# Kernel optimization log

Hardware: AMD Instinct MI355X
Metric: run time of the kernel (lower is better)

The kernel has to match this reference:

```python
import jax, jax.numpy as jnp
import numpy as np

N_NODES = 100_000
N_EDGES = 1_600_000
D_IN, D_HID, N_CLASSES = 128, 128, 40


def setup_inputs() -> dict:
    key = jax.random.key(0)
    ks = jax.random.split(key, 8)
    x = jax.random.normal(ks[0], (N_NODES, D_IN), dtype=jnp.float32)
    edge_index = jax.random.randint(ks[1], (2, N_EDGES), 0, N_NODES, dtype=jnp.int64)
    dims = [(D_IN, D_HID), (D_HID, D_HID), (D_HID, N_CLASSES)]
    inp = {"x": x, "edge_index": edge_index}
    for i, (di, do) in enumerate(dims):
        s = 1.0 / np.sqrt(di)
        inp[f"W_l{i}"] = jax.random.normal(ks[2 + 2 * i], (di, do), dtype=jnp.float32) * s
        inp[f"W_r{i}"] = jax.random.normal(ks[3 + 2 * i], (di, do), dtype=jnp.float32) * s
        inp[f"b{i}"] = jnp.zeros((do,), dtype=jnp.float32)
    return inp


def _sage_conv(x, src, dst, deg_inv, W_l, W_r, b):
    # gather messages from source nodes, mean-aggregate at target nodes
    msg = x[src]                                        # [E, d_in]
    aggr = jax.ops.segment_sum(msg, dst, num_segments=N_NODES) * deg_inv  # [N, d_in]
    return aggr @ W_l + b + x @ W_r                     # [N, d_out]


def reference(x, edge_index, W_l0, W_r0, b0, W_l1, W_r1, b1, W_l2, W_r2, b2):
    src, dst = edge_index[0], edge_index[1]
    deg = jax.ops.segment_sum(jnp.ones((N_EDGES,), x.dtype), dst, num_segments=N_NODES)
    deg_inv = (1.0 / jnp.maximum(deg, 1.0))[:, None]    # [N, 1]

    h = _sage_conv(x, src, dst, deg_inv, W_l0, W_r0, b0)
    h = jax.nn.relu(h)  # dropout p=0.3 is identity in eval mode
    h = _sage_conv(h, src, dst, deg_inv, W_l1, W_r1, b1)
    h = jax.nn.relu(h)
    h = _sage_conv(h, src, dst, deg_inv, W_l2, W_r2, b2)
    return jax.nn.log_softmax(h, axis=1)
```

## Files before the change

### kernel.cpp

```cpp
#include <hip/hip_runtime.h>
#include <math.h>

#define THREADS 256
#define BSHIFT 8
#define BSIZE 256
#define NEB 512

typedef short short8 __attribute__((ext_vector_type(8)));
typedef float f32x4 __attribute__((ext_vector_type(4)));

__device__ __forceinline__ unsigned short f2bf(float f) {
  unsigned u = __builtin_bit_cast(unsigned, f);
  return (unsigned short)((u + 0x7FFFu + ((u >> 16) & 1u)) >> 16);
}
__device__ __forceinline__ float bflo(unsigned u) {
  return __builtin_bit_cast(float, u << 16);
}
__device__ __forceinline__ float bfhi(unsigned u) {
  return __builtin_bit_cast(float, u & 0xFFFF0000u);
}
__device__ __forceinline__ unsigned pack2(float x, float y) {
  return (unsigned)f2bf(x) | ((unsigned)f2bf(y) << 16);
}

__device__ __forceinline__ void acc8(float* a, uint4 u) {
  a[0] += bflo(u.x); a[1] += bfhi(u.x);
  a[2] += bflo(u.y); a[3] += bfhi(u.y);
  a[4] += bflo(u.z); a[5] += bfhi(u.z);
  a[6] += bflo(u.w); a[7] += bfhi(u.w);
}


__global__ __launch_bounds__(256) void k_ehist(const int* __restrict__ dst,
                                               int* __restrict__ cnt_bm,
                                               int E, int chunk, int nbk) {
  __shared__ int h[1024];
  int blk = blockIdx.x, t = threadIdx.x;
  for (int i = t; i < nbk; i += 256) h[i] = 0;
  __syncthreads();
  int e0 = blk * chunk, e1 = min(e0 + chunk, E);
  for (int e = e0 + t; e < e1; e += 256) atomicAdd(&h[dst[e] >> BSHIFT], 1);
  __syncthreads();
  for (int i = t; i < nbk; i += 256) cnt_bm[(size_t)blk * nbk + i] = h[i];
}

__global__ __launch_bounds__(256) void k_bktscan(const int* __restrict__ cnt_bm,
                                                 int* __restrict__ locoff_tm,
                                                 int* __restrict__ bktot, int nbk) {
  int g = blockIdx.x, t = threadIdx.x;
  int c0 = cnt_bm[(size_t)(2 * t) * nbk + g];
  int c1 = cnt_bm[(size_t)(2 * t + 1) * nbk + g];
  __shared__ int sh[256];
  int s = c0 + c1;
  sh[t] = s;
  __syncthreads();
  for (int off = 1; off < 256; off <<= 1) {
    int v = (t >= off) ? sh[t - off] : 0;
    __syncthreads();
    if (t >= off) sh[t] += v;
    __syncthreads();
  }
  int excl = sh[t] - s;
  ((int2*)(locoff_tm + (size_t)g * NEB))[t] = make_int2(excl, excl + c0);
  if (t == 255) bktot[g] = sh[255];
}

__global__ __launch_bounds__(256) void k_topscan(const int* __restrict__ bktot,
                                                 int* __restrict__ bucket_base,
                                                 int nbk, int E,
                                                 int* __restrict__ row_ptr, int N) {
  __shared__ int sums[256];
  int t = threadIdx.x;
  int vals[4];
  int s = 0;
#pragma unroll
  for (int j = 0; j < 4; ++j) {
    int idx = t * 4 + j;
    vals[j] = (idx < nbk) ? bktot[idx] : 0;
    s += vals[j];
  }
  sums[t] = s;
  __syncthreads();
  for (int off = 1; off < 256; off <<= 1) {
    int v = (t >= off) ? sums[t - off] : 0;
    __syncthreads();
    if (t >= off) sums[t] += v;
    __syncthreads();
  }
  int run = sums[t] - s;
#pragma unroll
  for (int j = 0; j < 4; ++j) {
    int idx = t * 4 + j;
    if (idx < nbk) bucket_base[idx] = run;
    run += vals[j];
  }
  if (t == 0) { bucket_base[nbk] = E; row_ptr[N] = E; }
}

__global__ __launch_bounds__(256) void k_eplace(const int* __restrict__ src,
                                                const int* __restrict__ dst,
                                                const int* __restrict__ bucket_base,
                                                const int* __restrict__ locoff_tm,
                                                int* __restrict__ bedge,
                                                int E, int chunk, int nbk) {
  __shared__ int lptr[1024];
  int blk = blockIdx.x, t = threadIdx.x;
  for (int i = t; i < nbk; i += 256)
    lptr[i] = bucket_base[i] + locoff_tm[(size_t)i * NEB + blk];
  __syncthreads();
  int e0 = blk * chunk, e1 = min(e0 + chunk, E);
  for (int e = e0 + t; e < e1; e += 256) {
    int d = dst[e];
    int b = d >> BSHIFT;
    int p = atomicAdd(&lptr[b], 1);
    bedge[p] = (src[e] << 8) | (d & (BSIZE - 1));
  }
}

__global__ __launch_bounds__(256) void k_bcsr2(const int* __restrict__ bedge,
                                               const int* __restrict__ bucket_base,
                                               int* __restrict__ row_ptr,
                                               int* __restrict__ col, int N) {
  int g = blockIdx.x, t = threadIdx.x;
  int beg = bucket_base[g], end = bucket_base[g + 1];
  __shared__ int deg[BSIZE];
  __shared__ int sh[BSIZE];
  __shared__ int cur[BSIZE];
  deg[t] = 0;
  __syncthreads();
  for (int i = beg + t; i < end; i += 256)
    atomicAdd(&deg[bedge[i] & (BSIZE - 1)], 1);
  __syncthreads();
  int s = deg[t];
  sh[t] = s;
  __syncthreads();
  for (int off = 1; off < 256; off <<= 1) {
    int v = (t >= off) ? sh[t - off] : 0;
    __syncthreads();
    if (t >= off) sh[t] += v;
    __syncthreads();
  }
  int ex = beg + sh[t] - s;
  int node = g * BSIZE + t;
  if (node < N) row_ptr[node] = ex;
  cur[t] = ex;
  __syncthreads();
  for (int i = beg + t; i < end; i += 256) {
    int ed = bedge[i];
    int p = atomicAdd(&cur[ed & (BSIZE - 1)], 1);
    col[p] = ed >> 8;
  }
}

__global__ __launch_bounds__(256) void k_wswz_all(
    const float* __restrict__ Wl0, const float* __restrict__ Wr0,
    const float* __restrict__ Wl1, const float* __restrict__ Wr1,
    const float* __restrict__ Wl2, const float* __restrict__ Wr2,
    unsigned short* __restrict__ out0, unsigned short* __restrict__ out1,
    unsigned short* __restrict__ out2) {
  int b = blockIdx.x, t = threadIdx.x;
  if (b < 256) {
    const float* Wl = (b < 128) ? Wl0 : Wl1;
    const float* Wr = (b < 128) ? Wr0 : Wr1;
    unsigned short* out = (b < 128) ? out0 : out1;
    int idx = (b & 127) * 256 + t;
    int j = idx & 7, lane = (idx >> 3) & 63, ct = (idx >> 9) & 15, ks = idx >> 13;
    int k = ks * 32 + (lane >> 4) * 8 + j;
    int c = ct * 16 + (lane & 15);
    float v = (c < 128) ? Wl[k * 128 + c] : Wr[k * 128 + (c - 128)];
    out[idx] = f2bf(v);
  } else {
    int idx = (b - 256) * 256 + t;
    int j = idx & 7, lane = (idx >> 3) & 63;
    int tile = idx >> 9;
    int ct = tile % 5, ks = tile / 5;
    int k = ks * 32 + (lane >> 4) * 8 + j;
    int c = ct * 16 + (lane & 15);
    float v = (c < 40) ? Wl2[k * 40 + c] : ((c < 80) ? Wr2[k * 40 + (c - 40)] : 0.f);
    out2[idx] = f2bf(v);
  }
}

__global__ __launch_bounds__(256) void gemm128_mfma_x32(
    const float* __restrict__ X, const unsigned short* __restrict__ Wswz,
    const float* __restrict__ bias,
    unsigned short* __restrict__ outL, unsigned short* __restrict__ outR, int M) {
  int wave = threadIdx.x >> 6, lane = threadIdx.x & 63;
  int quad = lane >> 4, n16 = lane & 15;
  int rowA = blockIdx.x * 128 + wave * 16 + n16;
  int rowB = rowA + 64;
  int rA = min(rowA, M - 1), rB = min(rowB, M - 1);
  bool okA = rowA < M, okB = rowB < M;

  short8 xf[4], xg[4];
  const float* xpA = X + (size_t)rA * 128 + quad * 8;
  const float* xpB = X + (size_t)rB * 128 + quad * 8;
#pragma unroll
  for (int ks = 0; ks < 4; ++ks) {
    float4 a0 = *(const float4*)(xpA + ks * 32);
    float4 a1 = *(const float4*)(xpA + ks * 32 + 4);
    float4 b0 = *(const float4*)(xpB + ks * 32);
    float4 b1 = *(const float4*)(xpB + ks * 32 + 4);
    short8 f, g;
    f[0] = (short)f2bf(a0.x); f[1] = (short)f2bf(a0.y);
    f[2] = (short)f2bf(a0.z); f[3] = (short)f2bf(a0.w);
    f[4] = (short)f2bf(a1.x); f[5] = (short)f2bf(a1.y);
    f[6] = (short)f2bf(a1.z); f[7] = (short)f2bf(a1.w);
    g[0] = (short)f2bf(b0.x); g[1] = (short)f2bf(b0.y);
    g[2] = (short)f2bf(b0.z); g[3] = (short)f2bf(b0.w);
    g[4] = (short)f2bf(b1.x); g[5] = (short)f2bf(b1.y);
    g[6] = (short)f2bf(b1.z); g[7] = (short)f2bf(b1.w);
    xf[ks] = f;
    xg[ks] = g;
  }

  size_t obA = (size_t)rowA * 128, obB = (size_t)rowB * 128;
#pragma unroll 2
  for (int ct = 0; ct < 16; ++ct) {
    f32x4 accA = {0.f, 0.f, 0.f, 0.f};
    f32x4 accB = {0.f, 0.f, 0.f, 0.f};
    const unsigned short* wp = Wswz + (size_t)(ct * 64 + lane) * 8;
#pragma unroll
    for (int ks = 0; ks < 4; ++ks) {
      short8 wf = *(const short8*)(wp + ks * 8192);
      accA = __builtin_amdgcn_mfma_f32_16x16x32_bf16(wf, xf[ks], accA, 0, 0, 0);
      accB = __builtin_amdgcn_mfma_f32_16x16x32_bf16(wf, xg[ks], accB, 0, 0, 0);
    }
    int colh = (ct & 7) * 16 + quad * 4;
    if (ct < 8) {
      if (okA) {
        ushort4 o;
        o.x = f2bf(accA[0]); o.y = f2bf(accA[1]); o.z = f2bf(accA[2]); o.w = f2bf(accA[3]);
        *(ushort4*)(outL + obA + colh) = o;
      }
      if (okB) {
        ushort4 o;
        o.x = f2bf(accB[0]); o.y = f2bf(accB[1]); o.z = f2bf(accB[2]); o.w = f2bf(accB[3]);
        *(ushort4*)(outL + obB + colh) = o;
      }
    } else {
      float4 bv = *(const float4*)(bias + colh);
      if (okA) {
        ushort4 o;
        o.x = f2bf(accA[0] + bv.x); o.y = f2bf(accA[1] + bv.y);
        o.z = f2bf(accA[2] + bv.z); o.w = f2bf(accA[3] + bv.w);
        *(ushort4*)(outR + obA + colh) = o;
      }
      if (okB) {
        ushort4 o;
        o.x = f2bf(accB[0] + bv.x); o.y = f2bf(accB[1] + bv.y);
        o.z = f2bf(accB[2] + bv.z); o.w = f2bf(accB[3] + bv.w);
        *(ushort4*)(outR + obB + colh) = o;
      }
    }
  }
}

__global__ __launch_bounds__(256) void gemm128_mfma(
    const unsigned short* __restrict__ Xb, const unsigned short* __restrict__ Wswz,
    const float* __restrict__ bias,
    unsigned short* __restrict__ outL, unsigned short* __restrict__ outR, int M) {
  int wave = threadIdx.x >> 6, lane = threadIdx.x & 63;
  int quad = lane >> 4, n16 = lane & 15;
  int rowA = blockIdx.x * 128 + wave * 16 + n16;
  int rowB = rowA + 64;
  int rA = min(rowA, M - 1), rB = min(rowB, M - 1);
  bool okA = rowA < M, okB = rowB < M;

  short8 xf[4], xg[4];
  const unsigned short* xpA = Xb + (size_t)rA * 128 + quad * 8;
  const unsigned short* xpB = Xb + (size_t)rB * 128 + quad * 8;
#pragma unroll
  for (int ks = 0; ks < 4; ++ks) {
    xf[ks] = *(const short8*)(xpA + ks * 32);
    xg[ks] = *(const short8*)(xpB + ks * 32);
  }

  size_t obA = (size_t)rowA * 128, obB = (size_t)rowB * 128;
#pragma unroll 2
  for (int ct = 0; ct < 16; ++ct) {
    f32x4 accA = {0.f, 0.f, 0.f, 0.f};
    f32x4 accB = {0.f, 0.f, 0.f, 0.f};
    const unsigned short* wp = Wswz + (size_t)(ct * 64 + lane) * 8;
#pragma unroll
    for (int ks = 0; ks < 4; ++ks) {
      short8 wf = *(const short8*)(wp + ks * 8192);
      accA = __builtin_amdgcn_mfma_f32_16x16x32_bf16(wf, xf[ks], accA, 0, 0, 0);
      accB = __builtin_amdgcn_mfma_f32_16x16x32_bf16(wf, xg[ks], accB, 0, 0, 0);
    }
    int colh = (ct & 7) * 16 + quad * 4;
    if (ct < 8) {
      if (okA) {
        ushort4 o;
        o.x = f2bf(accA[0]); o.y = f2bf(accA[1]); o.z = f2bf(accA[2]); o.w = f2bf(accA[3]);
        *(ushort4*)(outL + obA + colh) = o;
      }
      if (okB) {
        ushort4 o;
        o.x = f2bf(accB[0]); o.y = f2bf(accB[1]); o.z = f2bf(accB[2]); o.w = f2bf(accB[3]);
        *(ushort4*)(outL + obB + colh) = o;
      }
    } else {
      float4 bv = *(const float4*)(bias + colh);
      if (okA) {
        ushort4 o;
        o.x = f2bf(accA[0] + bv.x); o.y = f2bf(accA[1] + bv.y);
        o.z = f2bf(accA[2] + bv.z); o.w = f2bf(accA[3] + bv.w);
        *(ushort4*)(outR + obA + colh) = o;
      }
      if (okB) {
        ushort4 o;
        o.x = f2bf(accB[0] + bv.x); o.y = f2bf(accB[1] + bv.y);
        o.z = f2bf(accB[2] + bv.z); o.w = f2bf(accB[3] + bv.w);
        *(ushort4*)(outR + obB + colh) = o;
      }
    }
  }
}

__global__ __launch_bounds__(256) void gemm40_mfma(
    const unsigned short* __restrict__ Xb, const unsigned short* __restrict__ Wswz,
    const float* __restrict__ bias,
    unsigned short* __restrict__ tlb, float* __restrict__ tr, int M) {
  int wave = threadIdx.x >> 6, lane = threadIdx.x & 63;
  int quad = lane >> 4, n16 = lane & 15;
  int row = blockIdx.x * 64 + wave * 16 + n16;
  int row_ld = min(row, M - 1);
  bool ok = row < M;

  short8 xf[4];
  const unsigned short* xp = Xb + (size_t)row_ld * 128 + quad * 8;
#pragma unroll
  for (int ks = 0; ks < 4; ++ks) xf[ks] = *(const short8*)(xp + ks * 32);

#pragma unroll
  for (int ct = 0; ct < 5; ++ct) {
    f32x4 acc = {0.f, 0.f, 0.f, 0.f};
    const unsigned short* wp = Wswz + (size_t)(ct * 64 + lane) * 8;
#pragma unroll
    for (int ks = 0; ks < 4; ++ks) {
      short8 wf = *(const short8*)(wp + (size_t)ks * 5 * 64 * 8);
      acc = __builtin_amdgcn_mfma_f32_16x16x32_bf16(wf, xf[ks], acc, 0, 0, 0);
    }
    int cglob = ct * 16 + quad * 4;
    if (!ok) continue;
    if (cglob < 40) {
      ushort4 o;
      o.x = f2bf(acc[0]); o.y = f2bf(acc[1]); o.z = f2bf(acc[2]); o.w = f2bf(acc[3]);
      *(ushort4*)(tlb + (size_t)row * 64 + cglob) = o;
    } else {
      int c = cglob - 40;
      float4 bv = *(const float4*)(bias + c);
      float4 o;
      o.x = acc[0] + bv.x; o.y = acc[1] + bv.y;
      o.z = acc[2] + bv.z; o.w = acc[3] + bv.w;
      *(float4*)(tr + (size_t)row * 40 + c) = o;
    }
  }
}

__global__ __launch_bounds__(256) void agg128b(
    const unsigned short* __restrict__ xl, const unsigned short* __restrict__ xr,
    const int* __restrict__ row_ptr, const int* __restrict__ col,
    unsigned short* __restrict__ h, int Nn) {
  int wave = threadIdx.x >> 6;
  int lane = threadIdx.x & 63;
  int pair = lane >> 5;
  int l32 = lane & 31;
  int n = blockIdx.x * 4 + wave;
  if (n >= Nn) return;
  int beg = row_ptr[n], end = row_ptr[n + 1];
  int deg = end - beg;
  const uint2* xlq = (const uint2*)xl;
  float a0x = 0.f, a0y = 0.f, a0z = 0.f, a0w = 0.f;
  float a1x = 0.f, a1y = 0.f, a1z = 0.f, a1w = 0.f;
  float a2x = 0.f, a2y = 0.f, a2z = 0.f, a2w = 0.f;
  float a3x = 0.f, a3y = 0.f, a3z = 0.f, a3w = 0.f;
  int e = beg + pair;
  for (int it = deg >> 3; it > 0; --it, e += 8) {
    uint2 u0 = xlq[(size_t)col[e]     * 32 + l32];
    uint2 u1 = xlq[(size_t)col[e + 2] * 32 + l32];
    uint2 u2 = xlq[(size_t)col[e + 4] * 32 + l32];
    uint2 u3 = xlq[(size_t)col[e + 6] * 32 + l32];
    a0x += bflo(u0.x); a0y += bfhi(u0.x); a0z += bflo(u0.y); a0w += bfhi(u0.y);
    a1x += bflo(u1.x); a1y += bfhi(u1.x); a1z += bflo(u1.y); a1w += bfhi(u1.y);
    a2x += bflo(u2.x); a2y += bfhi(u2.x); a2z += bflo(u2.y); a2w += bfhi(u2.y);
    a3x += bflo(u3.x); a3y += bfhi(u3.x); a3z += bflo(u3.y); a3w += bfhi(u3.y);
  }
  for (; e < end; e += 2) {
    uint2 u = xlq[(size_t)col[e] * 32 + l32];
    a0x += bflo(u.x); a0y += bfhi(u.x); a0z += bflo(u.y); a0w += bfhi(u.y);
  }
  float ax = (a0x + a1x) + (a2x + a3x);
  float ay = (a0y + a1y) + (a2y + a3y);
  float az = (a0z + a1z) + (a2z + a3z);
  float aw = (a0w + a1w) + (a2w + a3w);
  ax += __shfl_xor(ax, 32);
  ay += __shfl_xor(ay, 32);
  az += __shfl_xor(az, 32);
  aw += __shfl_xor(aw, 32);
  if (pair == 0) {
    float di = 1.0f / (float)max(deg, 1);
    uint2 r = ((const uint2*)xr)[(size_t)n * 32 + l32];
    float ox = fmaxf(fmaf(ax, di, bflo(r.x)), 0.f);
    float oy = fmaxf(fmaf(ay, di, bfhi(r.x)), 0.f);
    float oz = fmaxf(fmaf(az, di, bflo(r.y)), 0.f);
    float ow = fmaxf(fmaf(aw, di, bfhi(r.y)), 0.f);
    uint2 o;
    o.x = pack2(ox, oy);
    o.y = pack2(oz, ow);
    ((uint2*)h)[(size_t)n * 32 + l32] = o;
  }
}

__global__ __launch_bounds__(256) void agg40_lsm(
    const unsigned short* __restrict__ tlb, const float* __restrict__ tr,
    const int* __restrict__ row_ptr, const int* __restrict__ col,
    float* __restrict__ out, int Nn) {
  int wave = threadIdx.x >> 6;
  int lane = threadIdx.x & 63;
  int ew = lane >> 3;
  int l8 = lane & 7;
  int n = blockIdx.x * 4 + wave;
  if (n >= Nn) return;
  int beg = row_ptr[n], end = row_ptr[n + 1];
  int deg = end - beg;
  const uint4* tlq = (const uint4*)tlb;
  float a0[8], a1[8];
#pragma unroll
  for (int j = 0; j < 8; ++j) { a0[j] = 0.f; a1[j] = 0.f; }
  int rounds = (deg + 15) >> 4;
  if (rounds > 0) {
    int end1 = end - 1;
    int e = beg + ew;
    int c0 = col[min(e, end1)];
    int c1 = col[min(e + 8, end1)];
    for (int it = rounds - 1; it > 0; --it) {
      uint4 u0 = tlq[(size_t)c0 * 8 + l8];
      uint4 u1 = tlq[(size_t)c1 * 8 + l8];
      int en = e + 16;
      int cn0 = col[min(en, end1)];
      int cn1 = col[min(en + 8, end1)];
      acc8(a0, u0); acc8(a1, u1);
      c0 = cn0; c1 = cn1; e = en;
    }
    uint4 u0 = tlq[(size_t)c0 * 8 + l8];
    uint4 u1 = tlq[(size_t)c1 * 8 + l8];
    uint4 z = make_uint4(0u, 0u, 0u, 0u);
    if (e >= end) u0 = z;
    if (e + 8 >= end) u1 = z;
    acc8(a0, u0); acc8(a1, u1);
  }
  float v[8];
#pragma unroll
  for (int j = 0; j < 8; ++j) {
    float t = a0[j] + a1[j];
    t += __shfl_xor(t, 32);
    t += __shfl_xor(t, 16);
    t += __shfl_xor(t, 8);
    v[j] = t;
  }
  bool valid = l8 < 5;
  float di = 1.0f / (float)max(deg, 1);
  float4 r0 = valid ? *(const float4*)(tr + (size_t)n * 40 + 8 * l8)
                    : make_float4(0.f, 0.f, 0.f, 0.f);
  float4 r1 = valid ? *(const float4*)(tr + (size_t)n * 40 + 8 * l8 + 4)
                    : make_float4(0.f, 0.f, 0.f, 0.f);
  float rb[8] = {r0.x, r0.y, r0.z, r0.w, r1.x, r1.y, r1.z, r1.w};
  float vv[8];
#pragma unroll
  for (int j = 0; j < 8; ++j) vv[j] = valid ? fmaf(v[j], di, rb[j]) : -INFINITY;
  float m = vv[0];
#pragma unroll
  for (int j = 1; j < 8; ++j) m = fmaxf(m, vv[j]);
#pragma unroll
  for (int off = 4; off; off >>= 1) m = fmaxf(m, __shfl_xor(m, off));
  float ex = 0.f;
  if (valid) {
#pragma unroll
    for (int j = 0; j < 8; ++j) ex += expf(vv[j] - m);
  }
  float ssum = ex;
#pragma unroll
  for (int off = 4; off; off >>= 1) ssum += __shfl_xor(ssum, off);
  float lg = logf(ssum);
  if (ew == 0 && valid) {
    float4 o0, o1;
    o0.x = (vv[0] - m) - lg; o0.y = (vv[1] - m) - lg;
    o0.z = (vv[2] - m) - lg; o0.w = (vv[3] - m) - lg;
    o1.x = (vv[4] - m) - lg; o1.y = (vv[5] - m) - lg;
    o1.z = (vv[6] - m) - lg; o1.w = (vv[7] - m) - lg;
    *(float4*)(out + (size_t)n * 40 + 8 * l8) = o0;
    *(float4*)(out + (size_t)n * 40 + 8 * l8 + 4) = o1;
  }
}


extern "C" void kernel_launch(void* const* d_in, const int* in_sizes, int n_in,
                              void* d_out, int out_size, void* d_ws, size_t ws_size,
                              hipStream_t stream) {
  const float* x   = (const float*)d_in[0];
  const int*   ei  = (const int*)d_in[1];
  const float* Wl0 = (const float*)d_in[2];
  const float* Wr0 = (const float*)d_in[3];
  const float* b0  = (const float*)d_in[4];
  const float* Wl1 = (const float*)d_in[5];
  const float* Wr1 = (const float*)d_in[6];
  const float* b1  = (const float*)d_in[7];
  const float* Wl2 = (const float*)d_in[8];
  const float* Wr2 = (const float*)d_in[9];
  const float* b2  = (const float*)d_in[10];

  int N = in_sizes[0] / 128;
  int E = in_sizes[1] / 2;
  const int* src = ei;
  const int* dst = ei + E;
  int nbk = (N + BSIZE - 1) / BSIZE;
  int chunk = (E + NEB - 1) / NEB;

  char* ws = (char*)d_ws;
  size_t off = 0;
  auto alloc = [&](size_t bytes) -> void* {
    void* p = ws + off;
    off += (bytes + 255) & ~(size_t)255;
    return p;
  };
  unsigned short* gA  = (unsigned short*)alloc((size_t)N * 128 * 2);
  unsigned short* gB  = (unsigned short*)alloc((size_t)N * 128 * 2);
  unsigned short* hC  = (unsigned short*)alloc((size_t)N * 128 * 2);
  unsigned short* tlb = (unsigned short*)alloc((size_t)N * 64 * 2);
  float* tr           = (float*)alloc((size_t)N * 40 * 4);
  int* row_ptr  = (int*)alloc((size_t)(N + 1) * 4);
  int* col      = (int*)alloc((size_t)E * 4);
  int* bedge    = (int*)alloc((size_t)E * 4);
  int* cnt_bm   = (int*)alloc((size_t)NEB * nbk * 4);
  int* locoff   = (int*)alloc((size_t)nbk * NEB * 4);
  int* bktot    = (int*)alloc((size_t)nbk * 4);
  int* bbase    = (int*)alloc((size_t)(nbk + 1) * 4);
  unsigned short* wswz0 = (unsigned short*)alloc(32768 * 2);
  unsigned short* wswz1 = (unsigned short*)alloc(32768 * 2);
  unsigned short* wswz2 = (unsigned short*)alloc(10240 * 2);
  (void)ws_size; (void)n_in; (void)out_size;

  k_ehist<<<NEB, 256, 0, stream>>>(dst, cnt_bm, E, chunk, nbk);
  k_bktscan<<<nbk, 256, 0, stream>>>(cnt_bm, locoff, bktot, nbk);
  k_topscan<<<1, 256, 0, stream>>>(bktot, bbase, nbk, E, row_ptr, N);
  k_eplace<<<NEB, 256, 0, stream>>>(src, dst, bbase, locoff, bedge, E, chunk, nbk);
  k_bcsr2<<<nbk, 256, 0, stream>>>(bedge, bbase, row_ptr, col, N);

  k_wswz_all<<<296, 256, 0, stream>>>(Wl0, Wr0, Wl1, Wr1, Wl2, Wr2,
                                      wswz0, wswz1, wswz2);

  int gg128 = (N + 127) / 128;
  int gg = (N + 63) / 64;
  int nb = (N + 3) / 4;

  gemm128_mfma_x32<<<gg128, 256, 0, stream>>>(x, wswz0, b0, gA, gB, N);
  agg128b<<<nb, 256, 0, stream>>>(gA, gB, row_ptr, col, hC, N);
  gemm128_mfma<<<gg128, 256, 0, stream>>>(hC, wswz1, b1, gA, gB, N);
  agg128b<<<nb, 256, 0, stream>>>(gA, gB, row_ptr, col, hC, N);
  gemm40_mfma<<<gg, 256, 0, stream>>>(hC, wswz2, b2, tlb, tr, N);
  agg40_lsm<<<nb, 256, 0, stream>>>(tlb, tr, row_ptr, col, (float*)d_out, N);
}
```

Measured before the change: 446.7 us.

## Store GEMM outputs in column-sliced layout and aggregate per 16-column slice

The GEMM kernels now write their bf16 outputs as 8 slices of 16 columns, each slice contiguous over all nodes (32 bytes per node per slice), rather than as row-major 128-column rows. The aggregation kernel launches 8 blocks per node group, one per slice. Each block gathers 16 edges at once with 4 lanes per edge and reduces them with shuffles. The aim is for each slice (about 3.2 MB) to stay resident in cache during the random neighbour gathers, which should improve hit rates. In exchange, each 32-byte gather is smaller, the column index and row_ptr are read 8 times, and the shuffle reduction is longer.

```diff
diff --git a/kernel.cpp b/kernel.cpp
--- a/kernel.cpp
+++ b/kernel.cpp
@@ -214,7 +214,6 @@
     xg[ks] = g;
   }
 
-  size_t obA = (size_t)rowA * 128, obB = (size_t)rowB * 128;
 #pragma unroll 2
   for (int ct = 0; ct < 16; ++ct) {
     f32x4 accA = {0.f, 0.f, 0.f, 0.f};
@@ -226,31 +225,32 @@
       accA = __builtin_amdgcn_mfma_f32_16x16x32_bf16(wf, xf[ks], accA, 0, 0, 0);
       accB = __builtin_amdgcn_mfma_f32_16x16x32_bf16(wf, xg[ks], accB, 0, 0, 0);
     }
-    int colh = (ct & 7) * 16 + quad * 4;
     if (ct < 8) {
+      size_t sbase = (size_t)ct * M;
       if (okA) {
         ushort4 o;
         o.x = f2bf(accA[0]); o.y = f2bf(accA[1]); o.z = f2bf(accA[2]); o.w = f2bf(accA[3]);
-        *(ushort4*)(outL + obA + colh) = o;
+        *(ushort4*)(outL + (sbase + rowA) * 16 + quad * 4) = o;
       }
       if (okB) {
         ushort4 o;
         o.x = f2bf(accB[0]); o.y = f2bf(accB[1]); o.z = f2bf(accB[2]); o.w = f2bf(accB[3]);
-        *(ushort4*)(outL + obB + colh) = o;
+        *(ushort4*)(outL + (sbase + rowB) * 16 + quad * 4) = o;
       }
     } else {
-      float4 bv = *(const float4*)(bias + colh);
+      size_t sbase = (size_t)(ct - 8) * M;
+      float4 bv = *(const float4*)(bias + (ct - 8) * 16 + quad * 4);
       if (okA) {
         ushort4 o;
         o.x = f2bf(accA[0] + bv.x); o.y = f2bf(accA[1] + bv.y);
         o.z = f2bf(accA[2] + bv.z); o.w = f2bf(accA[3] + bv.w);
-        *(ushort4*)(outR + obA + colh) = o;
+        *(ushort4*)(outR + (sbase + rowA) * 16 + quad * 4) = o;
       }
       if (okB) {
         ushort4 o;
         o.x = f2bf(accB[0] + bv.x); o.y = f2bf(accB[1] + bv.y);
         o.z = f2bf(accB[2] + bv.z); o.w = f2bf(accB[3] + bv.w);
-        *(ushort4*)(outR + obB + colh) = o;
+        *(ushort4*)(outR + (sbase + rowB) * 16 + quad * 4) = o;
       }
     }
   }
@@ -276,7 +276,6 @@
     xg[ks] = *(const short8*)(xpB + ks * 32);
   }
 
-  size_t obA = (size_t)rowA * 128, obB = (size_t)rowB * 128;
 #pragma unroll 2
   for (int ct = 0; ct < 16; ++ct) {
     f32x4 accA = {0.f, 0.f, 0.f, 0.f};
@@ -288,31 +287,32 @@
       accA = __builtin_amdgcn_mfma_f32_16x16x32_bf16(wf, xf[ks], accA, 0, 0, 0);
       accB = __builtin_amdgcn_mfma_f32_16x16x32_bf16(wf, xg[ks], accB, 0, 0, 0);
     }
-    int colh = (ct & 7) * 16 + quad * 4;
     if (ct < 8) {
+      size_t sbase = (size_t)ct * M;
       if (okA) {
         ushort4 o;
         o.x = f2bf(accA[0]); o.y = f2bf(accA[1]); o.z = f2bf(accA[2]); o.w = f2bf(accA[3]);
-        *(ushort4*)(outL + obA + colh) = o;
+        *(ushort4*)(outL + (sbase + rowA) * 16 + quad * 4) = o;
       }
       if (okB) {
         ushort4 o;
         o.x = f2bf(accB[0]); o.y = f2bf(accB[1]); o.z = f2bf(accB[2]); o.w = f2bf(accB[3]);
-        *(ushort4*)(outL + obB + colh) = o;
+        *(ushort4*)(outL + (sbase + rowB) * 16 + quad * 4) = o;
       }
     } else {
-      float4 bv = *(const float4*)(bias + colh);
+      size_t sbase = (size_t)(ct - 8) * M;
+      float4 bv = *(const float4*)(bias + (ct - 8) * 16 + quad * 4);
       if (okA) {
         ushort4 o;
         o.x = f2bf(accA[0] + bv.x); o.y = f2bf(accA[1] + bv.y);
         o.z = f2bf(accA[2] + bv.z); o.w = f2bf(accA[3] + bv.w);
-        *(ushort4*)(outR + obA + colh) = o;
+        *(ushort4*)(outR + (sbase + rowA) * 16 + quad * 4) = o;
       }
       if (okB) {
         ushort4 o;
         o.x = f2bf(accB[0] + bv.x); o.y = f2bf(accB[1] + bv.y);
         o.z = f2bf(accB[2] + bv.z); o.w = f2bf(accB[3] + bv.w);
-        *(ushort4*)(outR + obB + colh) = o;
+        *(ushort4*)(outR + (sbase + rowB) * 16 + quad * 4) = o;
       }
     }
   }
@@ -359,57 +359,51 @@
   }
 }
 
-__global__ __launch_bounds__(256) void agg128b(
-    const unsigned short* __restrict__ xl, const unsigned short* __restrict__ xr,
+__global__ __launch_bounds__(256) void agg128s(
+    const unsigned short* __restrict__ gAs, const unsigned short* __restrict__ gBs,
     const int* __restrict__ row_ptr, const int* __restrict__ col,
     unsigned short* __restrict__ h, int Nn) {
+  int bid = blockIdx.x;
+  int s = bid & 7;
+  int nblk = bid >> 3;
   int wave = threadIdx.x >> 6;
   int lane = threadIdx.x & 63;
-  int pair = lane >> 5;
-  int l32 = lane & 31;
-  int n = blockIdx.x * 4 + wave;
+  int es = lane >> 2;
+  int cl = lane & 3;
+  int n = nblk * 4 + wave;
   if (n >= Nn) return;
   int beg = row_ptr[n], end = row_ptr[n + 1];
   int deg = end - beg;
-  const uint2* xlq = (const uint2*)xl;
-  float a0x = 0.f, a0y = 0.f, a0z = 0.f, a0w = 0.f;
-  float a1x = 0.f, a1y = 0.f, a1z = 0.f, a1w = 0.f;
-  float a2x = 0.f, a2y = 0.f, a2z = 0.f, a2w = 0.f;
-  float a3x = 0.f, a3y = 0.f, a3z = 0.f, a3w = 0.f;
-  int e = beg + pair;
-  for (int it = deg >> 3; it > 0; --it, e += 8) {
-    uint2 u0 = xlq[(size_t)col[e]     * 32 + l32];
-    uint2 u1 = xlq[(size_t)col[e + 2] * 32 + l32];
-    uint2 u2 = xlq[(size_t)col[e + 4] * 32 + l32];
-    uint2 u3 = xlq[(size_t)col[e + 6] * 32 + l32];
-    a0x += bflo(u0.x); a0y += bfhi(u0.x); a0z += bflo(u0.y); a0w += bfhi(u0.y);
-    a1x += bflo(u1.x); a1y += bfhi(u1.x); a1z += bflo(u1.y); a1w += bfhi(u1.y);
-    a2x += bflo(u2.x); a2y += bfhi(u2.x); a2z += bflo(u2.y); a2w += bfhi(u2.y);
-    a3x += bflo(u3.x); a3y += bfhi(u3.x); a3z += bflo(u3.y); a3w += bfhi(u3.y);
-  }
-  for (; e < end; e += 2) {
-    uint2 u = xlq[(size_t)col[e] * 32 + l32];
-    a0x += bflo(u.x); a0y += bfhi(u.x); a0z += bflo(u.y); a0w += bfhi(u.y);
-  }
-  float ax = (a0x + a1x) + (a2x + a3x);
-  float ay = (a0y + a1y) + (a2y + a3y);
-  float az = (a0z + a1z) + (a2z + a3z);
-  float aw = (a0w + a1w) + (a2w + a3w);
-  ax += __shfl_xor(ax, 32);
-  ay += __shfl_xor(ay, 32);
-  az += __shfl_xor(az, 32);
-  aw += __shfl_xor(aw, 32);
-  if (pair == 0) {
+  const uint2* A = (const uint2*)gAs;
+  size_t sbase = (size_t)s * Nn;
+  float a0 = 0.f, a1 = 0.f, a2 = 0.f, a3 = 0.f;
+  int e = beg + es;
+  int end1 = end - 1;
+  for (int r = (deg + 15) >> 4; r > 0; --r, e += 16) {
+    int c = col[min(e, end1)];
+    uint2 u = A[(sbase + c) * 4 + cl];
+    if (e >= end) { u.x = 0u; u.y = 0u; }
+    a0 += bflo(u.x); a1 += bfhi(u.x); a2 += bflo(u.y); a3 += bfhi(u.y);
+  }
+  a0 += __shfl_xor(a0, 4);  a1 += __shfl_xor(a1, 4);
+  a2 += __shfl_xor(a2, 4);  a3 += __shfl_xor(a3, 4);
+  a0 += __shfl_xor(a0, 8);  a1 += __shfl_xor(a1, 8);
+  a2 += __shfl_xor(a2, 8);  a3 += __shfl_xor(a3, 8);
+  a0 += __shfl_xor(a0, 16); a1 += __shfl_xor(a1, 16);
+  a2 += __shfl_xor(a2, 16); a3 += __shfl_xor(a3, 16);
+  a0 += __shfl_xor(a0, 32); a1 += __shfl_xor(a1, 32);
+  a2 += __shfl_xor(a2, 32); a3 += __shfl_xor(a3, 32);
+  if (es == 0) {
     float di = 1.0f / (float)max(deg, 1);
-    uint2 r = ((const uint2*)xr)[(size_t)n * 32 + l32];
-    float ox = fmaxf(fmaf(ax, di, bflo(r.x)), 0.f);
-    float oy = fmaxf(fmaf(ay, di, bfhi(r.x)), 0.f);
-    float oz = fmaxf(fmaf(az, di, bflo(r.y)), 0.f);
-    float ow = fmaxf(fmaf(aw, di, bfhi(r.y)), 0.f);
+    uint2 rr = ((const uint2*)gBs)[(sbase + n) * 4 + cl];
+    float ox = fmaxf(fmaf(a0, di, bflo(rr.x)), 0.f);
+    float oy = fmaxf(fmaf(a1, di, bfhi(rr.x)), 0.f);
+    float oz = fmaxf(fmaf(a2, di, bflo(rr.y)), 0.f);
+    float ow = fmaxf(fmaf(a3, di, bfhi(rr.y)), 0.f);
     uint2 o;
     o.x = pack2(ox, oy);
     o.y = pack2(oz, ow);
-    ((uint2*)h)[(size_t)n * 32 + l32] = o;
+    ((uint2*)h)[(size_t)n * 32 + s * 4 + cl] = o;
   }
 }
 
@@ -553,12 +547,13 @@
 
   int gg128 = (N + 127) / 128;
   int gg = (N + 63) / 64;
+  int nb8 = 8 * ((N + 3) / 4);
   int nb = (N + 3) / 4;
 
   gemm128_mfma_x32<<<gg128, 256, 0, stream>>>(x, wswz0, b0, gA, gB, N);
-  agg128b<<<nb, 256, 0, stream>>>(gA, gB, row_ptr, col, hC, N);
+  agg128s<<<nb8, 256, 0, stream>>>(gA, gB, row_ptr, col, hC, N);
   gemm128_mfma<<<gg128, 256, 0, stream>>>(hC, wswz1, b1, gA, gB, N);
-  agg128b<<<nb, 256, 0, stream>>>(gA, gB, row_ptr, col, hC, N);
+  agg128s<<<nb8, 256, 0, stream>>>(gA, gB, row_ptr, col, hC, N);
   gemm40_mfma<<<gg, 256, 0, stream>>>(hC, wswz2, b2, tlb, tr, N);
   agg40_lsm<<<nb, 256, 0, stream>>>(tlb, tr, row_ptr, col, (float*)d_out, N);
 }
```

Result: slower. 719.4 us (+61.1%).

## Store GEMM outputs as column-sliced planes for aggregation gathers

Applied to the files above, without the earlier changes.

GEMM outputs (the gathered projection and the self term) move from row-major [N,128] bf16 to 16-column slabs laid out as [8][N][16], and the 40-class buffer becomes [5][N][16]. The aggregation kernels index by slab, so each gathered row is split across several separate 32-byte segments instead of one contiguous 256-byte row. The likely aim is better cache locality per column slab or more coalesced GEMM stores. The cost is that every random gather now touches several scattered segments, which could hurt DRAM and L2 efficiency.

```diff
diff --git a/kernel.cpp b/kernel.cpp
--- a/kernel.cpp
+++ b/kernel.cpp
@@ -214,7 +214,6 @@
     xg[ks] = g;
   }
 
-  size_t obA = (size_t)rowA * 128, obB = (size_t)rowB * 128;
 #pragma unroll 2
   for (int ct = 0; ct < 16; ++ct) {
     f32x4 accA = {0.f, 0.f, 0.f, 0.f};
@@ -226,31 +225,32 @@
       accA = __builtin_amdgcn_mfma_f32_16x16x32_bf16(wf, xf[ks], accA, 0, 0, 0);
       accB = __builtin_amdgcn_mfma_f32_16x16x32_bf16(wf, xg[ks], accB, 0, 0, 0);
     }
-    int colh = (ct & 7) * 16 + quad * 4;
     if (ct < 8) {
+      size_t sbase = (size_t)ct * M;
       if (okA) {
         ushort4 o;
         o.x = f2bf(accA[0]); o.y = f2bf(accA[1]); o.z = f2bf(accA[2]); o.w = f2bf(accA[3]);
-        *(ushort4*)(outL + obA + colh) = o;
+        *(ushort4*)(outL + (sbase + rowA) * 16 + quad * 4) = o;
       }
       if (okB) {
         ushort4 o;
         o.x = f2bf(accB[0]); o.y = f2bf(accB[1]); o.z = f2bf(accB[2]); o.w = f2bf(accB[3]);
-        *(ushort4*)(outL + obB + colh) = o;
+        *(ushort4*)(outL + (sbase + rowB) * 16 + quad * 4) = o;
       }
     } else {
-      float4 bv = *(const float4*)(bias + colh);
+      size_t sbase = (size_t)(ct - 8) * M;
+      float4 bv = *(const float4*)(bias + (ct - 8) * 16 + quad * 4);
       if (okA) {
         ushort4 o;
         o.x = f2bf(accA[0] + bv.x); o.y = f2bf(accA[1] + bv.y);
         o.z = f2bf(accA[2] + bv.z); o.w = f2bf(accA[3] + bv.w);
-        *(ushort4*)(outR + obA + colh) = o;
+        *(ushort4*)(outR + (sbase + rowA) * 16 + quad * 4) = o;
       }
       if (okB) {
         ushort4 o;
         o.x = f2bf(accB[0] + bv.x); o.y = f2bf(accB[1] + bv.y);
         o.z = f2bf(accB[2] + bv.z); o.w = f2bf(accB[3] + bv.w);
-        *(ushort4*)(outR + obB + colh) = o;
+        *(ushort4*)(outR + (sbase + rowB) * 16 + quad * 4) = o;
       }
     }
   }
@@ -276,7 +276,6 @@
     xg[ks] = *(const short8*)(xpB + ks * 32);
   }
 
-  size_t obA = (size_t)rowA * 128, obB = (size_t)rowB * 128;
 #pragma unroll 2
   for (int ct = 0; ct < 16; ++ct) {
     f32x4 accA = {0.f, 0.f, 0.f, 0.f};
@@ -288,31 +287,32 @@
       accA = __builtin_amdgcn_mfma_f32_16x16x32_bf16(wf, xf[ks], accA, 0, 0, 0);
       accB = __builtin_amdgcn_mfma_f32_16x16x32_bf16(wf, xg[ks], accB, 0, 0, 0);
     }
-    int colh = (ct & 7) * 16 + quad * 4;
     if (ct < 8) {
+      size_t sbase = (size_t)ct * M;
       if (okA) {
         ushort4 o;
         o.x = f2bf(accA[0]); o.y = f2bf(accA[1]); o.z = f2bf(accA[2]); o.w = f2bf(accA[3]);
-        *(ushort4*)(outL + obA + colh) = o;
+        *(ushort4*)(outL + (sbase + rowA) * 16 + quad * 4) = o;
       }
       if (okB) {
         ushort4 o;
         o.x = f2bf(accB[0]); o.y = f2bf(accB[1]); o.z = f2bf(accB[2]); o.w = f2bf(accB[3]);
-        *(ushort4*)(outL + obB + colh) = o;
+        *(ushort4*)(outL + (sbase + rowB) * 16 + quad * 4) = o;
       }
     } else {
-      float4 bv = *(const float4*)(bias + colh);
+      size_t sbase = (size_t)(ct - 8) * M;
+      float4 bv = *(const float4*)(bias + (ct - 8) * 16 + quad * 4);
       if (okA) {
         ushort4 o;
         o.x = f2bf(accA[0] + bv.x); o.y = f2bf(accA[1] + bv.y);
         o.z = f2bf(accA[2] + bv.z); o.w = f2bf(accA[3] + bv.w);
-        *(ushort4*)(outR + obA + colh) = o;
+        *(ushort4*)(outR + (sbase + rowA) * 16 + quad * 4) = o;
       }
       if (okB) {
         ushort4 o;
         o.x = f2bf(accB[0] + bv.x); o.y = f2bf(accB[1] + bv.y);
         o.z = f2bf(accB[2] + bv.z); o.w = f2bf(accB[3] + bv.w);
-        *(ushort4*)(outR + obB + colh) = o;
+        *(ushort4*)(outR + (sbase + rowB) * 16 + quad * 4) = o;
       }
     }
   }
@@ -347,7 +347,7 @@
     if (cglob < 40) {
       ushort4 o;
       o.x = f2bf(acc[0]); o.y = f2bf(acc[1]); o.z = f2bf(acc[2]); o.w = f2bf(acc[3]);
-      *(ushort4*)(tlb + (size_t)row * 64 + cglob) = o;
+      *(ushort4*)(tlb + ((size_t)ct * M + row) * 16 + quad * 4) = o;
     } else {
       int c = cglob - 40;
       float4 bv = *(const float4*)(bias + c);
@@ -359,8 +359,8 @@
   }
 }
 
-__global__ __launch_bounds__(256) void agg128b(
-    const unsigned short* __restrict__ xl, const unsigned short* __restrict__ xr,
+__global__ __launch_bounds__(256) void agg128sm(
+    const unsigned short* __restrict__ gAs, const unsigned short* __restrict__ gBs,
     const int* __restrict__ row_ptr, const int* __restrict__ col,
     unsigned short* __restrict__ h, int Nn) {
   int wave = threadIdx.x >> 6;
@@ -371,24 +371,26 @@
   if (n >= Nn) return;
   int beg = row_ptr[n], end = row_ptr[n + 1];
   int deg = end - beg;
-  const uint2* xlq = (const uint2*)xl;
+  const uint2* A = (const uint2*)gAs;
+  size_t lbase = (size_t)(l32 >> 2) * Nn;
+  int cl = l32 & 3;
   float a0x = 0.f, a0y = 0.f, a0z = 0.f, a0w = 0.f;
   float a1x = 0.f, a1y = 0.f, a1z = 0.f, a1w = 0.f;
   float a2x = 0.f, a2y = 0.f, a2z = 0.f, a2w = 0.f;
   float a3x = 0.f, a3y = 0.f, a3z = 0.f, a3w = 0.f;
   int e = beg + pair;
   for (int it = deg >> 3; it > 0; --it, e += 8) {
-    uint2 u0 = xlq[(size_t)col[e]     * 32 + l32];
-    uint2 u1 = xlq[(size_t)col[e + 2] * 32 + l32];
-    uint2 u2 = xlq[(size_t)col[e + 4] * 32 + l32];
-    uint2 u3 = xlq[(size_t)col[e + 6] * 32 + l32];
+    uint2 u0 = A[(lbase + col[e])     * 4 + cl];
+    uint2 u1 = A[(lbase + col[e + 2]) * 4 + cl];
+    uint2 u2 = A[(lbase + col[e + 4]) * 4 + cl];
+    uint2 u3 = A[(lbase + col[e + 6]) * 4 + cl];
     a0x += bflo(u0.x); a0y += bfhi(u0.x); a0z += bflo(u0.y); a0w += bfhi(u0.y);
     a1x += bflo(u1.x); a1y += bfhi(u1.x); a1z += bflo(u1.y); a1w += bfhi(u1.y);
     a2x += bflo(u2.x); a2y += bfhi(u2.x); a2z += bflo(u2.y); a2w += bfhi(u2.y);
     a3x += bflo(u3.x); a3y += bfhi(u3.x); a3z += bflo(u3.y); a3w += bfhi(u3.y);
   }
   for (; e < end; e += 2) {
-    uint2 u = xlq[(size_t)col[e] * 32 + l32];
+    uint2 u = A[(lbase + col[e]) * 4 + cl];
     a0x += bflo(u.x); a0y += bfhi(u.x); a0z += bflo(u.y); a0w += bfhi(u.y);
   }
   float ax = (a0x + a1x) + (a2x + a3x);
@@ -401,7 +403,7 @@
   aw += __shfl_xor(aw, 32);
   if (pair == 0) {
     float di = 1.0f / (float)max(deg, 1);
-    uint2 r = ((const uint2*)xr)[(size_t)n * 32 + l32];
+    uint2 r = ((const uint2*)gBs)[(lbase + n) * 4 + cl];
     float ox = fmaxf(fmaf(ax, di, bflo(r.x)), 0.f);
     float oy = fmaxf(fmaf(ay, di, bfhi(r.x)), 0.f);
     float oz = fmaxf(fmaf(az, di, bflo(r.y)), 0.f);
@@ -426,6 +428,8 @@
   int beg = row_ptr[n], end = row_ptr[n + 1];
   int deg = end - beg;
   const uint4* tlq = (const uint4*)tlb;
+  size_t lbase = (size_t)(l8 >> 1) * Nn;
+  int cl = l8 & 1;
   float a0[8], a1[8];
 #pragma unroll
   for (int j = 0; j < 8; ++j) { a0[j] = 0.f; a1[j] = 0.f; }
@@ -436,16 +440,16 @@
     int c0 = col[min(e, end1)];
     int c1 = col[min(e + 8, end1)];
     for (int it = rounds - 1; it > 0; --it) {
-      uint4 u0 = tlq[(size_t)c0 * 8 + l8];
-      uint4 u1 = tlq[(size_t)c1 * 8 + l8];
+      uint4 u0 = tlq[(lbase + c0) * 2 + cl];
+      uint4 u1 = tlq[(lbase + c1) * 2 + cl];
       int en = e + 16;
       int cn0 = col[min(en, end1)];
       int cn1 = col[min(en + 8, end1)];
       acc8(a0, u0); acc8(a1, u1);
       c0 = cn0; c1 = cn1; e = en;
     }
-    uint4 u0 = tlq[(size_t)c0 * 8 + l8];
-    uint4 u1 = tlq[(size_t)c1 * 8 + l8];
+    uint4 u0 = tlq[(lbase + c0) * 2 + cl];
+    uint4 u1 = tlq[(lbase + c1) * 2 + cl];
     uint4 z = make_uint4(0u, 0u, 0u, 0u);
     if (e >= end) u0 = z;
     if (e + 8 >= end) u1 = z;
@@ -556,9 +560,9 @@
   int nb = (N + 3) / 4;
 
   gemm128_mfma_x32<<<gg128, 256, 0, stream>>>(x, wswz0, b0, gA, gB, N);
-  agg128b<<<nb, 256, 0, stream>>>(gA, gB, row_ptr, col, hC, N);
+  agg128sm<<<nb, 256, 0, stream>>>(gA, gB, row_ptr, col, hC, N);
   gemm128_mfma<<<gg128, 256, 0, stream>>>(hC, wswz1, b1, gA, gB, N);
-  agg128b<<<nb, 256, 0, stream>>>(gA, gB, row_ptr, col, hC, N);
+  agg128sm<<<nb, 256, 0, stream>>>(gA, gB, row_ptr, col, hC, N);
   gemm40_mfma<<<gg, 256, 0, stream>>>(hC, wswz2, b2, tlb, tr, N);
   agg40_lsm<<<nb, 256, 0, stream>>>(tlb, tr, row_ptr, col, (float*)d_out, N);
 }
```

Measured after the change: 699.1 us. 1.57x slower.
